# Performance work log

Measured on AMD Instinct MI355X. Metric: run time of the kernel, lower is better.

Reference implementation:

```python
import jax, jax.numpy as jnp
import numpy as np

FILTER_K = 100  # filter_K from __init__
NUM_CLASSES = 1000


def setup_inputs() -> dict:
    key = jax.random.key(0)
    ks = jax.random.split(key, 7)
    B, Din, D, C, N = 256, 2048, 512, NUM_CLASSES, 50000
    x = jax.random.normal(ks[0], (B, Din), jnp.float32)
    Wf = jax.random.normal(ks[1], (Din, D), jnp.float32) * 0.02
    Wc = jax.random.normal(ks[2], (C, D), jnp.float32) * 0.05
    bc = jax.random.normal(ks[3], (C,), jnp.float32) * 0.01
    supports_in = jax.random.normal(ks[4], (N, D), jnp.float32)
    ent_in = jax.random.uniform(ks[5], (N,), jnp.float32)
    labels_idx = jax.random.randint(ks[6], (N,), 0, C)
    return {"x": x, "Wf": Wf, "Wc": Wc, "bc": bc,
            "supports_in": supports_in, "ent_in": ent_in, "labels_idx": labels_idx}


def _softmax_entropy(logits):
    # -(softmax * log_softmax).sum(1), computed stably in one pass
    logp = jax.nn.log_softmax(logits, axis=1)
    return -(jnp.exp(logp) * logp).sum(axis=1)


def reference(x, Wf, Wc, bc, supports_in, ent_in, labels_idx):
    C = Wc.shape[0]
    z = x @ Wf                    # featurizer: [B, D]
    p = z @ Wc.T + bc             # classifier logits: [B, C]
    yhat = jax.nn.one_hot(jnp.argmax(p, axis=1), C, dtype=z.dtype)
    ent_new = _softmax_entropy(p)
    labels_in = jax.nn.one_hot(labels_idx, C, dtype=z.dtype)

    # grow support memory
    supports = jnp.concatenate([supports_in, z], axis=0)   # [M, D]
    labels = jnp.concatenate([labels_in, yhat], axis=0)    # [M, C]
    ent = jnp.concatenate([ent_in, ent_new], axis=0)       # [M]

    # select_supports: per-class keep FILTER_K lowest-entropy entries.
    # Torch gathers a variable-size subset; equivalent fixed-shape form is a
    # boolean mask (non-selected rows contribute zero to the weights matmul).
    y = jnp.argmax(labels, axis=1)
    M = ent.shape[0]
    order = jnp.lexsort((ent, y))            # sort by class, then entropy
    y_sorted = y[order]
    # rank of each entry within its class segment
    rank = jnp.arange(M) - jnp.searchsorted(y_sorted, y_sorted, side='left')
    mask = jnp.zeros((M,), bool).at[order].set(rank < FILTER_K)
    maskf = mask.astype(z.dtype)

    # normalize supports row-wise (F.normalize, eps=1e-12), then masked matmul
    s_norm = supports / jnp.maximum(
        jnp.linalg.norm(supports, axis=1, keepdims=True), 1e-12)
    weights = (s_norm * maskf[:, None]).T @ (labels * maskf[:, None])  # [D, C]
    weights = weights / jnp.maximum(
        jnp.linalg.norm(weights, axis=0, keepdims=True), 1e-12)
    return z @ weights            # [B, C]
```

## Files before the change

### kernel.cpp

```cpp
#include <hip/hip_runtime.h>
#include <hip/hip_bf16.h>
#include <math.h>

#define BB   256
#define DIN  2048
#define DD   512
#define CC   1000
#define NN   50000
#define MM   (NN + BB)
#define FILTER_K 100
#define SLOT 512
#define CSTRIDE 16

#define SK1  32
#define SKP  8

#define Z_OFF     0
#define CNT_OFF   (Z_OFF + BB*DD)
#define EI_OFF    (CNT_OFF + 1024*CSTRIDE)
#define WN_OFF    (EI_OFF + CC*SLOT*2)
#define ZP_OFF    (WN_OFF + CC*DD)
#define PP_OFF    (ZP_OFF + SK1*BB*DD)

__global__ __launch_bounds__(256, 2) void fused_scatter_gemm_ab(
    const float* __restrict__ A, const float* __restrict__ B,
    float* __restrict__ Cp,
    const int* __restrict__ labels_idx, const float* __restrict__ ent_in,
    int* __restrict__ cnt, float2* __restrict__ ei) {
  __shared__ float As[16][68];
  __shared__ float Bs[16][132];
  const int gbid = blockIdx.x, tid = threadIdx.x;
  if (gbid >= 512) {
    int m = (gbid - 512) * 256 + tid;
    if (m < NN) {
      int c = labels_idx[m];
      int pos = atomicAdd(&cnt[c * CSTRIDE], 1);
      if (pos < SLOT) {
        float2 pr; pr.x = ent_in[m]; pr.y = __int_as_float(m);
        ei[(size_t)c * SLOT + pos] = pr;
      }
    }
    return;
  }
  const int m0 = ((gbid >> 2) & 3) * 64;
  const int n0 = (gbid & 3) * 128;
  const int k0 = (gbid >> 4) * 64;
  const int ar = tid >> 2, ac = (tid & 3) * 4;
  const int br = tid >> 4, bcn = (tid & 15) * 8;
  const int tm = (tid >> 4) * 4, tn = (tid & 15) * 4;
  float acc[4][8] = {};
  float4 av  = *(const float4*)&A[(size_t)(m0 + ar) * DIN + k0 + ac];
  float4 bv0 = *(const float4*)&B[(size_t)(k0 + br) * DD + n0 + bcn];
  float4 bv1 = *(const float4*)&B[(size_t)(k0 + br) * DD + n0 + bcn + 4];
  for (int kk = 0; kk < 64; kk += 16) {
    __syncthreads();
    As[ac + 0][ar] = av.x; As[ac + 1][ar] = av.y;
    As[ac + 2][ar] = av.z; As[ac + 3][ar] = av.w;
    *(float4*)&Bs[br][bcn] = bv0;
    *(float4*)&Bs[br][bcn + 4] = bv1;
    __syncthreads();
    if (kk + 16 < 64) {
      av  = *(const float4*)&A[(size_t)(m0 + ar) * DIN + k0 + kk + 16 + ac];
      bv0 = *(const float4*)&B[(size_t)(k0 + kk + 16 + br) * DD + n0 + bcn];
      bv1 = *(const float4*)&B[(size_t)(k0 + kk + 16 + br) * DD + n0 + bcn + 4];
    }
#pragma unroll
    for (int q = 0; q < 16; ++q) {
      float4 a  = *(const float4*)&As[q][tm];
      float4 b0 = *(const float4*)&Bs[q][tn];
      float4 b1 = *(const float4*)&Bs[q][tn + 64];
      float aa[4] = {a.x, a.y, a.z, a.w};
      float bb[8] = {b0.x, b0.y, b0.z, b0.w, b1.x, b1.y, b1.z, b1.w};
#pragma unroll
      for (int i = 0; i < 4; ++i)
#pragma unroll
        for (int j = 0; j < 8; ++j) acc[i][j] += aa[i] * bb[j];
    }
  }
  float* Cb = Cp + (size_t)(gbid >> 4) * BB * DD;
#pragma unroll
  for (int i = 0; i < 4; ++i) {
    *(float4*)&Cb[(size_t)(m0 + tm + i) * DD + n0 + tn] =
        make_float4(acc[i][0], acc[i][1], acc[i][2], acc[i][3]);
    *(float4*)&Cb[(size_t)(m0 + tm + i) * DD + n0 + 64 + tn] =
        make_float4(acc[i][4], acc[i][5], acc[i][6], acc[i][7]);
  }
}

template <int S>
__global__ __launch_bounds__(256) void reduce_part(
    const float* __restrict__ part, float* __restrict__ out, int n4) {
  int i = blockIdx.x * 256 + threadIdx.x;
  if (i >= n4) return;
  const float4* p4 = (const float4*)part;
  float4 a = p4[i];
#pragma unroll
  for (int s = 1; s < S; ++s) {
    float4 b = p4[(size_t)s * n4 + i];
    a.x += b.x; a.y += b.y; a.z += b.z; a.w += b.w;
  }
  ((float4*)out)[i] = a;
}

__global__ __launch_bounds__(256, 2) void gemm_abt_part(
    const float* __restrict__ A, const float* __restrict__ Bm,
    float* __restrict__ Cp) {
  __shared__ float As[16][68];
  __shared__ float Bs[16][68];
  const int tid = threadIdx.x;
  const int m0 = blockIdx.y * 64;
  const int n0 = blockIdx.x * 64;
  const int k0 = blockIdx.z * 64;
  const int ar = tid >> 2, ac = (tid & 3) * 4;
  const int tm = (tid >> 4) * 4, tn = (tid & 15) * 4;
  float acc[4][4] = {};
  float4 av = *(const float4*)&A[(size_t)(m0 + ar) * DD + k0 + ac];
  float4 bv = make_float4(0.f, 0.f, 0.f, 0.f);
  if (n0 + ar < CC) bv = *(const float4*)&Bm[(size_t)(n0 + ar) * DD + k0 + ac];
  for (int kk = 0; kk < 64; kk += 16) {
    __syncthreads();
    As[ac + 0][ar] = av.x; As[ac + 1][ar] = av.y;
    As[ac + 2][ar] = av.z; As[ac + 3][ar] = av.w;
    Bs[ac + 0][ar] = bv.x; Bs[ac + 1][ar] = bv.y;
    Bs[ac + 2][ar] = bv.z; Bs[ac + 3][ar] = bv.w;
    __syncthreads();
    if (kk + 16 < 64) {
      av = *(const float4*)&A[(size_t)(m0 + ar) * DD + k0 + kk + 16 + ac];
      if (n0 + ar < CC)
        bv = *(const float4*)&Bm[(size_t)(n0 + ar) * DD + k0 + kk + 16 + ac];
    }
#pragma unroll
    for (int q = 0; q < 16; ++q) {
      float4 a = *(const float4*)&As[q][tm];
      float4 b = *(const float4*)&Bs[q][tn];
      float aa[4] = {a.x, a.y, a.z, a.w};
      float bb[4] = {b.x, b.y, b.z, b.w};
#pragma unroll
      for (int i = 0; i < 4; ++i)
#pragma unroll
        for (int j = 0; j < 4; ++j) acc[i][j] += aa[i] * bb[j];
    }
  }
  float* Cb = Cp + (size_t)blockIdx.z * BB * CC;
#pragma unroll
  for (int i = 0; i < 4; ++i) {
    int n = n0 + tn;
    if (n + 3 < CC) {
      *(float4*)&Cb[(size_t)(m0 + tm + i) * CC + n] =
          make_float4(acc[i][0], acc[i][1], acc[i][2], acc[i][3]);
    } else {
#pragma unroll
      for (int j = 0; j < 4; ++j)
        if (n + j < CC) Cb[(size_t)(m0 + tm + i) * CC + n + j] = acc[i][j];
    }
  }
}

__global__ __launch_bounds__(256) void rowstats(
    const float* __restrict__ ppart, const float* __restrict__ bc,
    int* __restrict__ cnt, float2* __restrict__ ei) {
  const int b = blockIdx.x, tid = threadIdx.x;
  const int lane = tid & 63, wid = tid >> 6;
  float r[4];
  float mv = -INFINITY; int mi = 0x7fffffff;
#pragma unroll
  for (int i = 0; i < 4; ++i) {
    int c = tid + 256 * i;
    if (c < CC) {
      float v = bc[c];
#pragma unroll
      for (int s = 0; s < SKP; ++s)
        v += ppart[(size_t)s * BB * CC + (size_t)b * CC + c];
      r[i] = v;
    } else r[i] = -INFINITY;
    if (r[i] > mv) { mv = r[i]; mi = c; }
  }
#pragma unroll
  for (int o = 32; o > 0; o >>= 1) {
    float ov = __shfl_down(mv, o, 64);
    int oi = __shfl_down(mi, o, 64);
    if (ov > mv || (ov == mv && oi < mi)) { mv = ov; mi = oi; }
  }
  __shared__ float smv[4]; __shared__ int smi[4];
  __shared__ float ssm[4], tsm[4];
  if (lane == 0) { smv[wid] = mv; smi[wid] = mi; }
  __syncthreads();
  if (tid == 0) {
#pragma unroll
    for (int w = 1; w < 4; ++w)
      if (smv[w] > smv[0] || (smv[w] == smv[0] && smi[w] < smi[0])) {
        smv[0] = smv[w]; smi[0] = smi[w];
      }
  }
  __syncthreads();
  const float m = smv[0]; const int am = smi[0];
  float s = 0.f, t = 0.f;
#pragma unroll
  for (int i = 0; i < 4; ++i) {
    if (tid + 256 * i < CC) {
      float u = r[i] - m;
      float e = expf(u);
      s += e; t += u * e;
    }
  }
#pragma unroll
  for (int o = 32; o > 0; o >>= 1) {
    s += __shfl_down(s, o, 64);
    t += __shfl_down(t, o, 64);
  }
  if (lane == 0) { ssm[wid] = s; tsm[wid] = t; }
  __syncthreads();
  if (tid == 0) {
    float S = ssm[0] + ssm[1] + ssm[2] + ssm[3];
    float T = tsm[0] + tsm[1] + tsm[2] + tsm[3];
    float ent = logf(S) - T / S;
    int pos = atomicAdd(&cnt[am * CSTRIDE], 1);
    if (pos < SLOT) {
      float2 pr; pr.x = ent; pr.y = __int_as_float(NN + b);
      ei[(size_t)am * SLOT + pos] = pr;
    }
  }
}

__global__ __launch_bounds__(256) void class_weights(
    const float* __restrict__ supports_in, const float* __restrict__ z,
    const float2* __restrict__ ei, const int* __restrict__ cnt,
    float* __restrict__ wn) {
  const int c = blockIdx.x, tid = threadIdx.x;
  const int lane = tid & 63, wid = tid >> 6;
  int n = cnt[c * CSTRIDE]; if (n > SLOT) n = SLOT;

  __shared__ int sel[SLOT];
  __shared__ float se[SLOT];
  __shared__ int si[SLOT];
  int seln;
  if (n <= FILTER_K) {
    seln = n;
    for (int i = tid; i < n; i += 256)
      sel[i] = __float_as_int(ei[(size_t)c * SLOT + i].y);
  } else {
    for (int i = tid; i < SLOT; i += 256) {
      if (i < n) {
        float2 pr = ei[(size_t)c * SLOT + i];
        se[i] = pr.x; si[i] = __float_as_int(pr.y);
      } else { se[i] = INFINITY; si[i] = 0x7fffffff; }
    }
    __syncthreads();
    for (int k = 2; k <= SLOT; k <<= 1)
      for (int j = k >> 1; j > 0; j >>= 1) {
        for (int i = tid; i < SLOT; i += 256) {
          int ixj = i ^ j;
          if (ixj > i) {
            bool up = ((i & k) == 0);
            float e1 = se[i], e2 = se[ixj];
            int i1 = si[i], i2 = si[ixj];
            bool gt = (e1 > e2) || (e1 == e2 && i1 > i2);
            if (gt == up) { se[i] = e2; se[ixj] = e1; si[i] = i2; si[ixj] = i1; }
          }
        }
        __syncthreads();
      }
    seln = FILTER_K;
    for (int i = tid; i < FILTER_K; i += 256) sel[i] = si[i];
  }
  __syncthreads();
  const int seln_pad = (seln + 15) & ~15;
  if (seln > 0)
    for (int i = seln + tid; i < seln_pad; i += 256) sel[i] = sel[0];
  __syncthreads();

  float4 a0 = make_float4(0.f, 0.f, 0.f, 0.f), a1 = a0;
  for (int t = wid * 4; t < seln_pad; t += 16) {
    float4 u0[4], u1[4]; float s[4];
#pragma unroll
    for (int j = 0; j < 4; ++j) {
      int r = sel[t + j];
      const float4* p4 = (const float4*)((r < NN)
          ? supports_in + (size_t)r * DD : z + (size_t)(r - NN) * DD);
      u0[j] = p4[lane * 2]; u1[j] = p4[lane * 2 + 1];
    }
#pragma unroll
    for (int j = 0; j < 4; ++j)
      s[j] = u0[j].x * u0[j].x + u0[j].y * u0[j].y + u0[j].z * u0[j].z
           + u0[j].w * u0[j].w + u1[j].x * u1[j].x + u1[j].y * u1[j].y
           + u1[j].z * u1[j].z + u1[j].w * u1[j].w;
#pragma unroll
    for (int o = 1; o < 64; o <<= 1) {
#pragma unroll
      for (int j = 0; j < 4; ++j) s[j] += __shfl_xor(s[j], o, 64);
    }
#pragma unroll
    for (int j = 0; j < 4; ++j) {
      float sc = (t + j < seln) ? 1.0f / fmaxf(sqrtf(s[j]), 1e-12f) : 0.f;
      a0.x += u0[j].x * sc; a0.y += u0[j].y * sc;
      a0.z += u0[j].z * sc; a0.w += u0[j].w * sc;
      a1.x += u1[j].x * sc; a1.y += u1[j].y * sc;
      a1.z += u1[j].z * sc; a1.w += u1[j].w * sc;
    }
  }

  __shared__ float part[4][DD];
  *(float4*)&part[wid][lane * 8] = a0;
  *(float4*)&part[wid][lane * 8 + 4] = a1;
  __syncthreads();
  const int d = tid * 2;
  float wx = part[0][d] + part[1][d] + part[2][d] + part[3][d];
  float wy = part[0][d + 1] + part[1][d + 1] + part[2][d + 1] + part[3][d + 1];
  float ss = wx * wx + wy * wy;
#pragma unroll
  for (int o = 1; o < 64; o <<= 1) ss += __shfl_xor(ss, o, 64);
  __shared__ float tot[4];
  if (lane == 0) tot[wid] = ss;
  __syncthreads();
  float S = tot[0] + tot[1] + tot[2] + tot[3];
  float sc = 1.0f / fmaxf(sqrtf(S), 1e-12f);
  ((float2*)(wn + (size_t)c * DD))[tid] = make_float2(wx * sc, wy * sc);
}

__global__ __launch_bounds__(256, 2) void gemm_out(
    const float* __restrict__ A, const float* __restrict__ Bm,
    float* __restrict__ C) {
  __shared__ float As[16][20];
  __shared__ float Bs[16][68];
  const int tid = threadIdx.x;
  const int m0 = blockIdx.y * 16;
  const int n0 = blockIdx.x * 64;
  const int arow = tid >> 4, ak = tid & 15;
  const int br = tid >> 2, bc = (tid & 3) * 4;
  const int tr = tid >> 4, tn4 = (tid & 15) * 4;
  float acc[4] = {};
  float av = A[(size_t)(m0 + arow) * DD + ak];
  float4 bv = make_float4(0.f, 0.f, 0.f, 0.f);
  if (n0 + br < CC) bv = *(const float4*)&Bm[(size_t)(n0 + br) * DD + bc];
  for (int k0 = 0; k0 < DD; k0 += 16) {
    __syncthreads();
    As[ak][arow] = av;
    Bs[bc + 0][br] = bv.x; Bs[bc + 1][br] = bv.y;
    Bs[bc + 2][br] = bv.z; Bs[bc + 3][br] = bv.w;
    __syncthreads();
    if (k0 + 16 < DD) {
      av = A[(size_t)(m0 + arow) * DD + k0 + 16 + ak];
      if (n0 + br < CC)
        bv = *(const float4*)&Bm[(size_t)(n0 + br) * DD + k0 + 16 + bc];
    }
#pragma unroll
    for (int q = 0; q < 16; ++q) {
      float a = As[q][tr];
      float4 b = *(const float4*)&Bs[q][tn4];
      acc[0] += a * b.x; acc[1] += a * b.y;
      acc[2] += a * b.z; acc[3] += a * b.w;
    }
  }
  int n = n0 + tn4;
  if (n + 3 < CC) {
    *(float4*)&C[(size_t)(m0 + tr) * CC + n] =
        make_float4(acc[0], acc[1], acc[2], acc[3]);
  } else {
#pragma unroll
    for (int j = 0; j < 4; ++j)
      if (n + j < CC) C[(size_t)(m0 + tr) * CC + n + j] = acc[j];
  }
}

extern "C" void kernel_launch(void* const* d_in, const int* in_sizes, int n_in,
                              void* d_out, int out_size, void* d_ws, size_t ws_size,
                              hipStream_t stream) {
  (void)in_sizes; (void)n_in; (void)out_size; (void)ws_size;
  const float* x           = (const float*)d_in[0];
  const float* Wf          = (const float*)d_in[1];
  const float* Wc          = (const float*)d_in[2];
  const float* bc          = (const float*)d_in[3];
  const float* supports_in = (const float*)d_in[4];
  const float* ent_in      = (const float*)d_in[5];
  const int*   labels_idx  = (const int*)d_in[6];
  float* out = (float*)d_out;

  float* W = (float*)d_ws;
  float*  z     = W + Z_OFF;
  int*    cnt   = (int*)(W + CNT_OFF);
  float2* ei    = (float2*)(W + EI_OFF);
  float*  wn    = W + WN_OFF;
  float*  zpart = W + ZP_OFF;
  float*  ppart = W + PP_OFF;

  hipMemsetAsync(cnt, 0, 1024 * CSTRIDE * sizeof(int), stream);
  fused_scatter_gemm_ab<<<512 + (NN + 255) / 256, 256, 0, stream>>>(
      x, Wf, zpart, labels_idx, ent_in, cnt, ei);
  reduce_part<SK1><<<(BB * DD / 4 + 255) / 256, 256, 0, stream>>>(
      zpart, z, BB * DD / 4);
  gemm_abt_part<<<dim3((CC + 63) / 64, BB / 64, SKP), 256, 0, stream>>>(
      z, Wc, ppart);
  rowstats<<<BB, 256, 0, stream>>>(ppart, bc, cnt, ei);
  class_weights<<<CC, 256, 0, stream>>>(supports_in, z, ei, cnt, wn);
  gemm_out<<<dim3((CC + 63) / 64, BB / 16), 256, 0, stream>>>(z, wn, out);
}
```

Baseline: 219.8 us.

## Fuse all stages into one persistent kernel with software grid barriers

Replaces six kernel launches with a single persistent kernel of 512 blocks that runs each stage in turn, separated by atomic-counter grid barriers. The first GEMM's split-K factor is halved so 256 blocks cover it while the remaining blocks do the label scatter. The aim is to remove per-launch overhead and inter-kernel gaps. In exchange, stages that use fewer blocks leave others idle at each barrier, the barrier spin-waits add their own latency, and correctness relies on all 512 blocks being resident at once.

```diff
diff --git a/kernel.cpp b/kernel.cpp
--- a/kernel.cpp
+++ b/kernel.cpp
@@ -1,5 +1,4 @@
 #include <hip/hip_runtime.h>
-#include <hip/hip_bf16.h>
 #include <math.h>
 
 #define BB   256
@@ -7,13 +6,13 @@
 #define DD   512
 #define CC   1000
 #define NN   50000
-#define MM   (NN + BB)
 #define FILTER_K 100
 #define SLOT 512
 #define CSTRIDE 16
 
-#define SK1  32
+#define SK1  16
 #define SKP  8
+#define NBLK 512
 
 #define Z_OFF     0
 #define CNT_OFF   (Z_OFF + BB*DD)
@@ -22,217 +21,38 @@
 #define ZP_OFF    (WN_OFF + CC*DD)
 #define PP_OFF    (ZP_OFF + SK1*BB*DD)
 
-__global__ __launch_bounds__(256, 2) void fused_scatter_gemm_ab(
-    const float* __restrict__ A, const float* __restrict__ B,
-    float* __restrict__ Cp,
-    const int* __restrict__ labels_idx, const float* __restrict__ ent_in,
-    int* __restrict__ cnt, float2* __restrict__ ei) {
-  __shared__ float As[16][68];
-  __shared__ float Bs[16][132];
-  const int gbid = blockIdx.x, tid = threadIdx.x;
-  if (gbid >= 512) {
-    int m = (gbid - 512) * 256 + tid;
-    if (m < NN) {
-      int c = labels_idx[m];
-      int pos = atomicAdd(&cnt[c * CSTRIDE], 1);
-      if (pos < SLOT) {
-        float2 pr; pr.x = ent_in[m]; pr.y = __int_as_float(m);
-        ei[(size_t)c * SLOT + pos] = pr;
-      }
-    }
-    return;
-  }
-  const int m0 = ((gbid >> 2) & 3) * 64;
-  const int n0 = (gbid & 3) * 128;
-  const int k0 = (gbid >> 4) * 64;
-  const int ar = tid >> 2, ac = (tid & 3) * 4;
-  const int br = tid >> 4, bcn = (tid & 15) * 8;
-  const int tm = (tid >> 4) * 4, tn = (tid & 15) * 4;
-  float acc[4][8] = {};
-  float4 av  = *(const float4*)&A[(size_t)(m0 + ar) * DIN + k0 + ac];
-  float4 bv0 = *(const float4*)&B[(size_t)(k0 + br) * DD + n0 + bcn];
-  float4 bv1 = *(const float4*)&B[(size_t)(k0 + br) * DD + n0 + bcn + 4];
-  for (int kk = 0; kk < 64; kk += 16) {
-    __syncthreads();
-    As[ac + 0][ar] = av.x; As[ac + 1][ar] = av.y;
-    As[ac + 2][ar] = av.z; As[ac + 3][ar] = av.w;
-    *(float4*)&Bs[br][bcn] = bv0;
-    *(float4*)&Bs[br][bcn + 4] = bv1;
-    __syncthreads();
-    if (kk + 16 < 64) {
-      av  = *(const float4*)&A[(size_t)(m0 + ar) * DIN + k0 + kk + 16 + ac];
-      bv0 = *(const float4*)&B[(size_t)(k0 + kk + 16 + br) * DD + n0 + bcn];
-      bv1 = *(const float4*)&B[(size_t)(k0 + kk + 16 + br) * DD + n0 + bcn + 4];
-    }
-#pragma unroll
-    for (int q = 0; q < 16; ++q) {
-      float4 a  = *(const float4*)&As[q][tm];
-      float4 b0 = *(const float4*)&Bs[q][tn];
-      float4 b1 = *(const float4*)&Bs[q][tn + 64];
-      float aa[4] = {a.x, a.y, a.z, a.w};
-      float bb[8] = {b0.x, b0.y, b0.z, b0.w, b1.x, b1.y, b1.z, b1.w};
-#pragma unroll
-      for (int i = 0; i < 4; ++i)
-#pragma unroll
-        for (int j = 0; j < 8; ++j) acc[i][j] += aa[i] * bb[j];
-    }
-  }
-  float* Cb = Cp + (size_t)(gbid >> 4) * BB * DD;
-#pragma unroll
-  for (int i = 0; i < 4; ++i) {
-    *(float4*)&Cb[(size_t)(m0 + tm + i) * DD + n0 + tn] =
-        make_float4(acc[i][0], acc[i][1], acc[i][2], acc[i][3]);
-    *(float4*)&Cb[(size_t)(m0 + tm + i) * DD + n0 + 64 + tn] =
-        make_float4(acc[i][4], acc[i][5], acc[i][6], acc[i][7]);
-  }
+#define BAR_CNT_IDX  (1008*CSTRIDE)
+#define BAR_FLAG_IDX (1012*CSTRIDE)
+
+#define SMEM_F 3712
+
+__device__ __forceinline__ void gsync(int* bcnt, int* bflag, int epoch) {
+  __syncthreads();
+  if (threadIdx.x == 0) {
+    __threadfence();
+    int t = atomicAdd(bcnt, 1);
+    if (t == epoch * NBLK - 1) {
+      __hip_atomic_store(bflag, epoch, __ATOMIC_RELEASE, __HIP_MEMORY_SCOPE_AGENT);
+    } else {
+      while (__hip_atomic_load(bflag, __ATOMIC_ACQUIRE, __HIP_MEMORY_SCOPE_AGENT) < epoch)
+        __builtin_amdgcn_s_sleep(4);
+    }
+    __threadfence();
+  }
+  __syncthreads();
 }
 
-template <int S>
-__global__ __launch_bounds__(256) void reduce_part(
-    const float* __restrict__ part, float* __restrict__ out, int n4) {
-  int i = blockIdx.x * 256 + threadIdx.x;
-  if (i >= n4) return;
-  const float4* p4 = (const float4*)part;
-  float4 a = p4[i];
-#pragma unroll
-  for (int s = 1; s < S; ++s) {
-    float4 b = p4[(size_t)s * n4 + i];
-    a.x += b.x; a.y += b.y; a.z += b.z; a.w += b.w;
-  }
-  ((float4*)out)[i] = a;
-}
-
-__global__ __launch_bounds__(256, 2) void gemm_abt_part(
-    const float* __restrict__ A, const float* __restrict__ Bm,
-    float* __restrict__ Cp) {
-  __shared__ float As[16][68];
-  __shared__ float Bs[16][68];
-  const int tid = threadIdx.x;
-  const int m0 = blockIdx.y * 64;
-  const int n0 = blockIdx.x * 64;
-  const int k0 = blockIdx.z * 64;
-  const int ar = tid >> 2, ac = (tid & 3) * 4;
-  const int tm = (tid >> 4) * 4, tn = (tid & 15) * 4;
-  float acc[4][4] = {};
-  float4 av = *(const float4*)&A[(size_t)(m0 + ar) * DD + k0 + ac];
-  float4 bv = make_float4(0.f, 0.f, 0.f, 0.f);
-  if (n0 + ar < CC) bv = *(const float4*)&Bm[(size_t)(n0 + ar) * DD + k0 + ac];
-  for (int kk = 0; kk < 64; kk += 16) {
-    __syncthreads();
-    As[ac + 0][ar] = av.x; As[ac + 1][ar] = av.y;
-    As[ac + 2][ar] = av.z; As[ac + 3][ar] = av.w;
-    Bs[ac + 0][ar] = bv.x; Bs[ac + 1][ar] = bv.y;
-    Bs[ac + 2][ar] = bv.z; Bs[ac + 3][ar] = bv.w;
-    __syncthreads();
-    if (kk + 16 < 64) {
-      av = *(const float4*)&A[(size_t)(m0 + ar) * DD + k0 + kk + 16 + ac];
-      if (n0 + ar < CC)
-        bv = *(const float4*)&Bm[(size_t)(n0 + ar) * DD + k0 + kk + 16 + ac];
-    }
-#pragma unroll
-    for (int q = 0; q < 16; ++q) {
-      float4 a = *(const float4*)&As[q][tm];
-      float4 b = *(const float4*)&Bs[q][tn];
-      float aa[4] = {a.x, a.y, a.z, a.w};
-      float bb[4] = {b.x, b.y, b.z, b.w};
-#pragma unroll
-      for (int i = 0; i < 4; ++i)
-#pragma unroll
-        for (int j = 0; j < 4; ++j) acc[i][j] += aa[i] * bb[j];
-    }
-  }
-  float* Cb = Cp + (size_t)blockIdx.z * BB * CC;
-#pragma unroll
-  for (int i = 0; i < 4; ++i) {
-    int n = n0 + tn;
-    if (n + 3 < CC) {
-      *(float4*)&Cb[(size_t)(m0 + tm + i) * CC + n] =
-          make_float4(acc[i][0], acc[i][1], acc[i][2], acc[i][3]);
-    } else {
-#pragma unroll
-      for (int j = 0; j < 4; ++j)
-        if (n + j < CC) Cb[(size_t)(m0 + tm + i) * CC + n + j] = acc[i][j];
-    }
-  }
-}
-
-__global__ __launch_bounds__(256) void rowstats(
-    const float* __restrict__ ppart, const float* __restrict__ bc,
-    int* __restrict__ cnt, float2* __restrict__ ei) {
-  const int b = blockIdx.x, tid = threadIdx.x;
-  const int lane = tid & 63, wid = tid >> 6;
-  float r[4];
-  float mv = -INFINITY; int mi = 0x7fffffff;
-#pragma unroll
-  for (int i = 0; i < 4; ++i) {
-    int c = tid + 256 * i;
-    if (c < CC) {
-      float v = bc[c];
-#pragma unroll
-      for (int s = 0; s < SKP; ++s)
-        v += ppart[(size_t)s * BB * CC + (size_t)b * CC + c];
-      r[i] = v;
-    } else r[i] = -INFINITY;
-    if (r[i] > mv) { mv = r[i]; mi = c; }
-  }
-#pragma unroll
-  for (int o = 32; o > 0; o >>= 1) {
-    float ov = __shfl_down(mv, o, 64);
-    int oi = __shfl_down(mi, o, 64);
-    if (ov > mv || (ov == mv && oi < mi)) { mv = ov; mi = oi; }
-  }
-  __shared__ float smv[4]; __shared__ int smi[4];
-  __shared__ float ssm[4], tsm[4];
-  if (lane == 0) { smv[wid] = mv; smi[wid] = mi; }
-  __syncthreads();
-  if (tid == 0) {
-#pragma unroll
-    for (int w = 1; w < 4; ++w)
-      if (smv[w] > smv[0] || (smv[w] == smv[0] && smi[w] < smi[0])) {
-        smv[0] = smv[w]; smi[0] = smi[w];
-      }
-  }
-  __syncthreads();
-  const float m = smv[0]; const int am = smi[0];
-  float s = 0.f, t = 0.f;
-#pragma unroll
-  for (int i = 0; i < 4; ++i) {
-    if (tid + 256 * i < CC) {
-      float u = r[i] - m;
-      float e = expf(u);
-      s += e; t += u * e;
-    }
-  }
-#pragma unroll
-  for (int o = 32; o > 0; o >>= 1) {
-    s += __shfl_down(s, o, 64);
-    t += __shfl_down(t, o, 64);
-  }
-  if (lane == 0) { ssm[wid] = s; tsm[wid] = t; }
-  __syncthreads();
-  if (tid == 0) {
-    float S = ssm[0] + ssm[1] + ssm[2] + ssm[3];
-    float T = tsm[0] + tsm[1] + tsm[2] + tsm[3];
-    float ent = logf(S) - T / S;
-    int pos = atomicAdd(&cnt[am * CSTRIDE], 1);
-    if (pos < SLOT) {
-      float2 pr; pr.x = ent; pr.y = __int_as_float(NN + b);
-      ei[(size_t)am * SLOT + pos] = pr;
-    }
-  }
-}
-
-__global__ __launch_bounds__(256) void class_weights(
-    const float* __restrict__ supports_in, const float* __restrict__ z,
-    const float2* __restrict__ ei, const int* __restrict__ cnt,
-    float* __restrict__ wn) {
-  const int c = blockIdx.x, tid = threadIdx.x;
+__device__ __forceinline__ void do_class(
+    int c, int tid, float* smem, const float* supports_in, const float* z,
+    const float2* ei, const int* cnt, float* wn) {
+  int*   sel = (int*)smem;
+  float* se  = smem + SLOT;
+  int*   si  = (int*)(smem + 2*SLOT);
+  float (*part)[DD] = (float(*)[DD])(smem + 3*SLOT);
+  float* tot = smem + 3*SLOT + 4*DD;
   const int lane = tid & 63, wid = tid >> 6;
   int n = cnt[c * CSTRIDE]; if (n > SLOT) n = SLOT;
 
-  __shared__ int sel[SLOT];
-  __shared__ float se[SLOT];
-  __shared__ int si[SLOT];
   int seln;
   if (n <= FILTER_K) {
     seln = n;
@@ -299,7 +119,6 @@
     }
   }
 
-  __shared__ float part[4][DD];
   *(float4*)&part[wid][lane * 8] = a0;
   *(float4*)&part[wid][lane * 8 + 4] = a1;
   __syncthreads();
@@ -309,7 +128,6 @@
   float ss = wx * wx + wy * wy;
 #pragma unroll
   for (int o = 1; o < 64; o <<= 1) ss += __shfl_xor(ss, o, 64);
-  __shared__ float tot[4];
   if (lane == 0) tot[wid] = ss;
   __syncthreads();
   float S = tot[0] + tot[1] + tot[2] + tot[3];
@@ -317,48 +135,260 @@
   ((float2*)(wn + (size_t)c * DD))[tid] = make_float2(wx * sc, wy * sc);
 }
 
-__global__ __launch_bounds__(256, 2) void gemm_out(
-    const float* __restrict__ A, const float* __restrict__ Bm,
-    float* __restrict__ C) {
-  __shared__ float As[16][20];
-  __shared__ float Bs[16][68];
-  const int tid = threadIdx.x;
-  const int m0 = blockIdx.y * 16;
-  const int n0 = blockIdx.x * 64;
-  const int arow = tid >> 4, ak = tid & 15;
-  const int br = tid >> 2, bc = (tid & 3) * 4;
-  const int tr = tid >> 4, tn4 = (tid & 15) * 4;
-  float acc[4] = {};
-  float av = A[(size_t)(m0 + arow) * DD + ak];
-  float4 bv = make_float4(0.f, 0.f, 0.f, 0.f);
-  if (n0 + br < CC) bv = *(const float4*)&Bm[(size_t)(n0 + br) * DD + bc];
-  for (int k0 = 0; k0 < DD; k0 += 16) {
+__global__ __launch_bounds__(256, 2) void mega(
+    const float* x, const float* Wf, const float* Wc, const float* bc,
+    const float* supports_in, const float* ent_in, const int* labels_idx,
+    float* out, float* ws) {
+  __shared__ __align__(16) float smem[SMEM_F];
+  float*  z     = ws + Z_OFF;
+  int*    cnt   = (int*)(ws + CNT_OFF);
+  float2* ei    = (float2*)(ws + EI_OFF);
+  float*  wn    = ws + WN_OFF;
+  float*  zpart = ws + ZP_OFF;
+  float*  ppart = ws + PP_OFF;
+  int* bar_cnt  = cnt + BAR_CNT_IDX;
+  int* bar_flag = cnt + BAR_FLAG_IDX;
+  const int bid = blockIdx.x, tid = threadIdx.x;
+
+  if (bid < 256) {
+    float (*As)[68]  = (float(*)[68])smem;
+    float (*Bs)[132] = (float(*)[132])(smem + 16 * 68);
+    const int m0 = ((bid >> 2) & 3) * 64;
+    const int n0 = (bid & 3) * 128;
+    const int k0 = (bid >> 4) * 128;
+    const int ar = tid >> 2, ac = (tid & 3) * 4;
+    const int br = tid >> 4, bcn = (tid & 15) * 8;
+    const int tm = (tid >> 4) * 4, tn = (tid & 15) * 4;
+    float acc[4][8] = {};
+    float4 av  = *(const float4*)&x[(size_t)(m0 + ar) * DIN + k0 + ac];
+    float4 bv0 = *(const float4*)&Wf[(size_t)(k0 + br) * DD + n0 + bcn];
+    float4 bv1 = *(const float4*)&Wf[(size_t)(k0 + br) * DD + n0 + bcn + 4];
+    for (int kk = 0; kk < 128; kk += 16) {
+      __syncthreads();
+      As[ac + 0][ar] = av.x; As[ac + 1][ar] = av.y;
+      As[ac + 2][ar] = av.z; As[ac + 3][ar] = av.w;
+      *(float4*)&Bs[br][bcn] = bv0;
+      *(float4*)&Bs[br][bcn + 4] = bv1;
+      __syncthreads();
+      if (kk + 16 < 128) {
+        av  = *(const float4*)&x[(size_t)(m0 + ar) * DIN + k0 + kk + 16 + ac];
+        bv0 = *(const float4*)&Wf[(size_t)(k0 + kk + 16 + br) * DD + n0 + bcn];
+        bv1 = *(const float4*)&Wf[(size_t)(k0 + kk + 16 + br) * DD + n0 + bcn + 4];
+      }
+#pragma unroll
+      for (int q = 0; q < 16; ++q) {
+        float4 a  = *(const float4*)&As[q][tm];
+        float4 b0 = *(const float4*)&Bs[q][tn];
+        float4 b1 = *(const float4*)&Bs[q][tn + 64];
+        float aa[4] = {a.x, a.y, a.z, a.w};
+        float bb[8] = {b0.x, b0.y, b0.z, b0.w, b1.x, b1.y, b1.z, b1.w};
+#pragma unroll
+        for (int i = 0; i < 4; ++i)
+#pragma unroll
+          for (int j = 0; j < 8; ++j) acc[i][j] += aa[i] * bb[j];
+      }
+    }
+    float* Cb = zpart + (size_t)(bid >> 4) * BB * DD;
+#pragma unroll
+    for (int i = 0; i < 4; ++i) {
+      *(float4*)&Cb[(size_t)(m0 + tm + i) * DD + n0 + tn] =
+          make_float4(acc[i][0], acc[i][1], acc[i][2], acc[i][3]);
+      *(float4*)&Cb[(size_t)(m0 + tm + i) * DD + n0 + 64 + tn] =
+          make_float4(acc[i][4], acc[i][5], acc[i][6], acc[i][7]);
+    }
+  } else if (bid < 452) {
+    int m = (bid - 256) * 256 + tid;
+    if (m < NN) {
+      int c = labels_idx[m];
+      int pos = atomicAdd(&cnt[c * CSTRIDE], 1);
+      if (pos < SLOT) {
+        float2 pr; pr.x = ent_in[m]; pr.y = __int_as_float(m);
+        ei[(size_t)c * SLOT + pos] = pr;
+      }
+    }
+  }
+  gsync(bar_cnt, bar_flag, 1);
+
+  {
+    const int n4 = BB * DD / 4;
+    int i = bid * 256 + tid;
+    if (i < n4) {
+      const float4* p4 = (const float4*)zpart;
+      float4 a = p4[i];
+#pragma unroll
+      for (int s = 1; s < SK1; ++s) {
+        float4 b = p4[(size_t)s * n4 + i];
+        a.x += b.x; a.y += b.y; a.z += b.z; a.w += b.w;
+      }
+      ((float4*)z)[i] = a;
+    }
+  }
+  gsync(bar_cnt, bar_flag, 2);
+
+  {
+    float (*As)[68] = (float(*)[68])smem;
+    float (*Bs)[68] = (float(*)[68])(smem + 16 * 68);
+    const int n0 = (bid & 15) * 64;
+    const int m0 = ((bid >> 4) & 3) * 64;
+    const int ks = bid >> 6;
+    const int k0 = ks * 64;
+    const int ar = tid >> 2, ac = (tid & 3) * 4;
+    const int tm = (tid >> 4) * 4, tn = (tid & 15) * 4;
+    float acc[4][4] = {};
+    float4 av = *(const float4*)&z[(size_t)(m0 + ar) * DD + k0 + ac];
+    float4 bv = make_float4(0.f, 0.f, 0.f, 0.f);
+    if (n0 + ar < CC) bv = *(const float4*)&Wc[(size_t)(n0 + ar) * DD + k0 + ac];
+    for (int kk = 0; kk < 64; kk += 16) {
+      __syncthreads();
+      As[ac + 0][ar] = av.x; As[ac + 1][ar] = av.y;
+      As[ac + 2][ar] = av.z; As[ac + 3][ar] = av.w;
+      Bs[ac + 0][ar] = bv.x; Bs[ac + 1][ar] = bv.y;
+      Bs[ac + 2][ar] = bv.z; Bs[ac + 3][ar] = bv.w;
+      __syncthreads();
+      if (kk + 16 < 64) {
+        av = *(const float4*)&z[(size_t)(m0 + ar) * DD + k0 + kk + 16 + ac];
+        if (n0 + ar < CC)
+          bv = *(const float4*)&Wc[(size_t)(n0 + ar) * DD + k0 + kk + 16 + ac];
+      }
+#pragma unroll
+      for (int q = 0; q < 16; ++q) {
+        float4 a = *(const float4*)&As[q][tm];
+        float4 b = *(const float4*)&Bs[q][tn];
+        float aa[4] = {a.x, a.y, a.z, a.w};
+        float bb[4] = {b.x, b.y, b.z, b.w};
+#pragma unroll
+        for (int i = 0; i < 4; ++i)
+#pragma unroll
+          for (int j = 0; j < 4; ++j) acc[i][j] += aa[i] * bb[j];
+      }
+    }
+    float* Cb = ppart + (size_t)ks * BB * CC;
+#pragma unroll
+    for (int i = 0; i < 4; ++i) {
+      int n = n0 + tn;
+      if (n + 3 < CC) {
+        *(float4*)&Cb[(size_t)(m0 + tm + i) * CC + n] =
+            make_float4(acc[i][0], acc[i][1], acc[i][2], acc[i][3]);
+      } else {
+#pragma unroll
+        for (int j = 0; j < 4; ++j)
+          if (n + j < CC) Cb[(size_t)(m0 + tm + i) * CC + n + j] = acc[i][j];
+      }
+    }
+  }
+  gsync(bar_cnt, bar_flag, 3);
+
+  if (bid < BB) {
+    float* smv = smem; int* smi = (int*)(smem + 4);
+    float* ssm = smem + 8; float* tsm = smem + 12;
+    const int b = bid;
+    const int lane = tid & 63, wid = tid >> 6;
+    float r[4];
+    float mv = -INFINITY; int mi = 0x7fffffff;
+#pragma unroll
+    for (int i = 0; i < 4; ++i) {
+      int c = tid + 256 * i;
+      if (c < CC) {
+        float v = bc[c];
+#pragma unroll
+        for (int s = 0; s < SKP; ++s)
+          v += ppart[(size_t)s * BB * CC + (size_t)b * CC + c];
+        r[i] = v;
+      } else r[i] = -INFINITY;
+      if (r[i] > mv) { mv = r[i]; mi = c; }
+    }
+#pragma unroll
+    for (int o = 32; o > 0; o >>= 1) {
+      float ov = __shfl_down(mv, o, 64);
+      int oi = __shfl_down(mi, o, 64);
+      if (ov > mv || (ov == mv && oi < mi)) { mv = ov; mi = oi; }
+    }
+    if (lane == 0) { smv[wid] = mv; smi[wid] = mi; }
     __syncthreads();
-    As[ak][arow] = av;
-    Bs[bc + 0][br] = bv.x; Bs[bc + 1][br] = bv.y;
-    Bs[bc + 2][br] = bv.z; Bs[bc + 3][br] = bv.w;
+    if (tid == 0) {
+#pragma unroll
+      for (int w = 1; w < 4; ++w)
+        if (smv[w] > smv[0] || (smv[w] == smv[0] && smi[w] < smi[0])) {
+          smv[0] = smv[w]; smi[0] = smi[w];
+        }
+    }
     __syncthreads();
-    if (k0 + 16 < DD) {
-      av = A[(size_t)(m0 + arow) * DD + k0 + 16 + ak];
-      if (n0 + br < CC)
-        bv = *(const float4*)&Bm[(size_t)(n0 + br) * DD + k0 + 16 + bc];
-    }
-#pragma unroll
-    for (int q = 0; q < 16; ++q) {
-      float a = As[q][tr];
-      float4 b = *(const float4*)&Bs[q][tn4];
-      acc[0] += a * b.x; acc[1] += a * b.y;
-      acc[2] += a * b.z; acc[3] += a * b.w;
-    }
-  }
-  int n = n0 + tn4;
-  if (n + 3 < CC) {
-    *(float4*)&C[(size_t)(m0 + tr) * CC + n] =
-        make_float4(acc[0], acc[1], acc[2], acc[3]);
-  } else {
-#pragma unroll
-    for (int j = 0; j < 4; ++j)
-      if (n + j < CC) C[(size_t)(m0 + tr) * CC + n + j] = acc[j];
+    const float m = smv[0]; const int am = smi[0];
+    float s = 0.f, t = 0.f;
+#pragma unroll
+    for (int i = 0; i < 4; ++i) {
+      if (tid + 256 * i < CC) {
+        float u = r[i] - m;
+        float e = expf(u);
+        s += e; t += u * e;
+      }
+    }
+#pragma unroll
+    for (int o = 32; o > 0; o >>= 1) {
+      s += __shfl_down(s, o, 64);
+      t += __shfl_down(t, o, 64);
+    }
+    if (lane == 0) { ssm[wid] = s; tsm[wid] = t; }
+    __syncthreads();
+    if (tid == 0) {
+      float S = ssm[0] + ssm[1] + ssm[2] + ssm[3];
+      float T = tsm[0] + tsm[1] + tsm[2] + tsm[3];
+      float ent = logf(S) - T / S;
+      int pos = atomicAdd(&cnt[am * CSTRIDE], 1);
+      if (pos < SLOT) {
+        float2 pr; pr.x = ent; pr.y = __int_as_float(NN + b);
+        ei[(size_t)am * SLOT + pos] = pr;
+      }
+    }
+  }
+  gsync(bar_cnt, bar_flag, 4);
+
+  do_class(bid, tid, smem, supports_in, z, ei, cnt, wn);
+  __syncthreads();
+  if (bid + 512 < CC)
+    do_class(bid + 512, tid, smem, supports_in, z, ei, cnt, wn);
+  gsync(bar_cnt, bar_flag, 5);
+
+  if (bid < 256) {
+    float (*As)[20] = (float(*)[20])smem;
+    float (*Bs)[68] = (float(*)[68])(smem + 16 * 20);
+    const int m0 = (bid >> 4) * 16;
+    const int n0 = (bid & 15) * 64;
+    const int arow = tid >> 4, ak = tid & 15;
+    const int br = tid >> 2, bcl = (tid & 3) * 4;
+    const int tr = tid >> 4, tn4 = (tid & 15) * 4;
+    float acc[4] = {};
+    float av = z[(size_t)(m0 + arow) * DD + ak];
+    float4 bv = make_float4(0.f, 0.f, 0.f, 0.f);
+    if (n0 + br < CC) bv = *(const float4*)&wn[(size_t)(n0 + br) * DD + bcl];
+    for (int k0 = 0; k0 < DD; k0 += 16) {
+      __syncthreads();
+      As[ak][arow] = av;
+      Bs[bcl + 0][br] = bv.x; Bs[bcl + 1][br] = bv.y;
+      Bs[bcl + 2][br] = bv.z; Bs[bcl + 3][br] = bv.w;
+      __syncthreads();
+      if (k0 + 16 < DD) {
+        av = z[(size_t)(m0 + arow) * DD + k0 + 16 + ak];
+        if (n0 + br < CC)
+          bv = *(const float4*)&wn[(size_t)(n0 + br) * DD + k0 + 16 + bcl];
+      }
+#pragma unroll
+      for (int q = 0; q < 16; ++q) {
+        float a = As[q][tr];
+        float4 b = *(const float4*)&Bs[q][tn4];
+        acc[0] += a * b.x; acc[1] += a * b.y;
+        acc[2] += a * b.z; acc[3] += a * b.w;
+      }
+    }
+    int n = n0 + tn4;
+    if (n + 3 < CC) {
+      *(float4*)&out[(size_t)(m0 + tr) * CC + n] =
+          make_float4(acc[0], acc[1], acc[2], acc[3]);
+    } else {
+#pragma unroll
+      for (int j = 0; j < 4; ++j)
+        if (n + j < CC) out[(size_t)(m0 + tr) * CC + n + j] = acc[j];
+    }
   }
 }
 
@@ -374,23 +404,10 @@
   const float* ent_in      = (const float*)d_in[5];
   const int*   labels_idx  = (const int*)d_in[6];
   float* out = (float*)d_out;
-
   float* W = (float*)d_ws;
-  float*  z     = W + Z_OFF;
-  int*    cnt   = (int*)(W + CNT_OFF);
-  float2* ei    = (float2*)(W + EI_OFF);
-  float*  wn    = W + WN_OFF;
-  float*  zpart = W + ZP_OFF;
-  float*  ppart = W + PP_OFF;
+  int* cnt = (int*)(W + CNT_OFF);
 
   hipMemsetAsync(cnt, 0, 1024 * CSTRIDE * sizeof(int), stream);
-  fused_scatter_gemm_ab<<<512 + (NN + 255) / 256, 256, 0, stream>>>(
-      x, Wf, zpart, labels_idx, ent_in, cnt, ei);
-  reduce_part<SK1><<<(BB * DD / 4 + 255) / 256, 256, 0, stream>>>(
-      zpart, z, BB * DD / 4);
-  gemm_abt_part<<<dim3((CC + 63) / 64, BB / 64, SKP), 256, 0, stream>>>(
-      z, Wc, ppart);
-  rowstats<<<BB, 256, 0, stream>>>(ppart, bc, cnt, ei);
-  class_weights<<<CC, 256, 0, stream>>>(supports_in, z, ei, cnt, wn);
-  gemm_out<<<dim3((CC + 63) / 64, BB / 16), 256, 0, stream>>>(z, wn, out);
+  hipLaunchKernelGGL(mega, dim3(NBLK), dim3(256), 0, stream,
+                     x, Wf, Wc, bc, supports_in, ent_in, labels_idx, out, W);
 }
```

Result: slower. 425.9 us (+93.8%).
